# Optimization experiments

Hardware: AMD Instinct MI355X
Metric: run time of the kernel (lower is better)

The kernel has to match this reference:

```python
import jax, jax.numpy as jnp
import numpy as np

BINS = 100
ALPHA = 0.1

def entropy_batch(h):
    # Faithful to torch: histogram path is detached (done in numpy in original).
    h = jax.lax.stop_gradient(h)
    B, D = h.shape
    hp = h - jnp.min(h, axis=1, keepdims=True)
    hn = hp / jnp.max(hp, axis=1, keepdims=True)  # normalized to [0, 1]
    # np.histogram with `bins` uniform bins over [0,1]; rightmost edge inclusive -> clip
    idx = jnp.clip(jnp.floor(hn * BINS).astype(jnp.int32), 0, BINS - 1)
    rows = jnp.arange(B)[:, None]
    counts = jnp.zeros((B, BINS), jnp.float32).at[rows, idx].add(1.0)
    px = counts / jnp.float32(D)
    safe = jnp.where(px > 0, px, 1.0)
    ent = -jnp.sum(px * jnp.log(safe), axis=1) + jnp.log(jnp.float32(BINS))
    return jnp.mean(ent)

def setup_inputs() -> dict:
    key = jax.random.key(0)
    ks = jax.random.split(key, 8)
    B = 65536
    archi = [246, 246, 246, 246, 246, 246]
    dims = [784] + archi
    inp = {"x": jax.random.normal(ks[0], (B, 1, 28, 28), jnp.float32)}
    for i in range(6):
        inp[f"W{i+1}"] = 0.01 * jax.random.normal(ks[i + 1], (dims[i + 1], dims[i]), jnp.float32)
        inp[f"b{i+1}"] = jnp.zeros((dims[i + 1],), jnp.float32)
    inp["W7"] = 0.01 * jax.random.normal(ks[7], (10, archi[-1]), jnp.float32)
    inp["b7"] = jnp.zeros((10,), jnp.float32)
    return inp

def reference(x, W1, b1, W2, b2, W3, b3, W4, b4, W5, b5, W6, b6, W7, b7):
    h = x.reshape(-1, 784)
    Hs = []
    for W, b in ((W1, b1), (W2, b2), (W3, b3), (W4, b4), (W5, b5), (W6, b6)):
        h = jax.nn.leaky_relu(h @ W.T + b, negative_slope=ALPHA)
        Hs.append(entropy_batch(h))
    logits = jax.nn.relu(h @ W7.T + b7)
    out = jax.nn.log_softmax(logits, axis=1)
    return (out, Hs[0], Hs[1], Hs[2], Hs[3], Hs[4], Hs[5])
```

## Files before the change

kernel.cpp:

```cpp
#include <hip/hip_runtime.h>
#include <cstdint>
#include <cmath>

#define BATCH 65536
#define NREAL 246
#define NPAD  256
#define K1    784
#define K1PAD 832
#define BINS  100
#define ALPHA 0.1f
#define RB    32
#define NBLK  (BATCH/RB)

typedef __bf16 bf16x8 __attribute__((ext_vector_type(8)));
typedef __bf16 bf16x4 __attribute__((ext_vector_type(4)));
typedef float  f32x4  __attribute__((ext_vector_type(4)));

#define OFF_HS     0
#define OFF_STAGE  16384
#define OFF_HIST   16384
#define OFF_MN     29184
#define OFF_MX     29696
#define OFF_LUT    30208
#define OFF_WENT   31232
#define LDS_TOTAL  31328

__global__ __launch_bounds__(256)
void pad_weights(const float* __restrict__ W1, const float* __restrict__ W2,
                 const float* __restrict__ W3, const float* __restrict__ W4,
                 const float* __restrict__ W5, const float* __restrict__ W6,
                 const float* __restrict__ W7,
                 __bf16* __restrict__ W1p, __bf16* __restrict__ Wp,
                 __bf16* __restrict__ W7p)
{
    int tid = blockIdx.x * 256 + threadIdx.x;
    const int n1 = NPAD * K1PAD;
    const int n2 = 5 * NPAD * NPAD;
    if (tid < n1) {
        int row = tid / K1PAD;
        int k   = tid - row * K1PAD;
        W1p[tid] = (__bf16)((row < NREAL && k < K1) ? W1[row * K1 + k] : 0.0f);
    } else if (tid < n1 + n2) {
        int t = tid - n1;
        int wsel = t >> 16;
        int idx  = t & 65535;
        int row  = idx >> 8, k = idx & 255;
        const float* W = (wsel == 0) ? W2 : (wsel == 1) ? W3 : (wsel == 2) ? W4
                        : (wsel == 3) ? W5 : W6;
        Wp[t] = (__bf16)((row < NREAL && k < NREAL) ? W[row * NREAL + k] : 0.0f);
    } else if (tid < n1 + n2 + 16 * NPAD) {
        int t = tid - n1 - n2;
        int row = t >> 8, k = t & 255;
        W7p[t] = (__bf16)((row < 10 && k < NREAL) ? W7[row * NREAL + k] : 0.0f);
    }
}

__global__ __launch_bounds__(256)
void mega(const float* __restrict__ x,
          const __bf16* __restrict__ W1p,
          const __bf16* __restrict__ Wp,
          const __bf16* __restrict__ W7p,
          const float* __restrict__ b1, const float* __restrict__ b2,
          const float* __restrict__ b3, const float* __restrict__ b4,
          const float* __restrict__ b5, const float* __restrict__ b6,
          const float* __restrict__ b7,
          float* __restrict__ out, float* __restrict__ partial)
{
    __shared__ char smem[LDS_TOTAL];
    char*  Hb    = smem + OFF_HS;
    float* rowmn = (float*)(smem + OFF_MN);
    float* rowmx = (float*)(smem + OFF_MX);
    float* lut   = (float*)(smem + OFF_LUT);
    float* went  = (float*)(smem + OFF_WENT);

    const int tid = threadIdx.x;
    const int w = tid >> 6, l = tid & 63;
    const int lane16 = l & 15, lane4 = l >> 4;
    const int m0 = blockIdx.x * RB;

    if (tid > 0 && tid < 247) lut[tid] = (float)tid * logf((float)tid);
    if (tid == 0) lut[0] = 0.0f;

    f32x4 acc[2][4];
#pragma unroll
    for (int i = 0; i < 2; ++i)
#pragma unroll
        for (int j = 0; j < 4; ++j) acc[i][j] = f32x4{0.f, 0.f, 0.f, 0.f};

    auto loadBh = [&](bf16x8 (&dst)[4], const __bf16* Bbase, int Kb, int kt, int kk) {
        const __bf16* p = Bbase + (size_t)(w * 64 + lane16) * Kb + kt * 64 + kk * 32 + lane4 * 8;
#pragma unroll
        for (int j = 0; j < 4; ++j)
            dst[j] = *(const bf16x8*)(p + (size_t)j * 16 * Kb);
    };

    auto computeHalf = [&](const char* Ab, int rowStride, int kbyte, const bf16x8 (&bfr)[4]) {
#pragma unroll
        for (int i = 0; i < 2; ++i) {
            int row = i * 16 + lane16;
            bf16x8 af = *(const bf16x8*)(Ab + row * rowStride + ((kbyte + lane4 * 16) ^ ((row & 7) << 4)));
            __builtin_amdgcn_s_setprio(1);
#pragma unroll
            for (int j = 0; j < 4; ++j)
                acc[i][j] = __builtin_amdgcn_mfma_f32_16x16x32_bf16(af, bfr[j], acc[i][j], 0, 0, 0);
            __builtin_amdgcn_s_setprio(0);
        }
    };

    auto epilogue = [&](const float* bias) {
        float bv[4];
#pragma unroll
        for (int j = 0; j < 4; ++j) {
            int col = w * 64 + j * 16 + lane16;
            bv[j] = (col < NREAL) ? bias[col] : 0.0f;
        }
#pragma unroll
        for (int i = 0; i < 2; ++i) {
#pragma unroll
            for (int rr = 0; rr < 4; ++rr) {
                int row = i * 16 + lane4 * 4 + rr;
                int swz = (row & 7) << 4;
                float mn = 1e30f, mx = -1e30f;
#pragma unroll
                for (int j = 0; j < 4; ++j) {
                    int col = w * 64 + j * 16 + lane16;
                    bool cv = col < NREAL;
                    float v = acc[i][j][rr] + bv[j];
                    v = v > 0.0f ? v : ALPHA * v;
                    *(__bf16*)(Hb + row * 512 + ((col * 2) ^ swz)) = cv ? (__bf16)v : (__bf16)0.0f;
                    mn = fminf(mn, cv ? v : 1e30f);
                    mx = fmaxf(mx, cv ? v : -1e30f);
                }
#pragma unroll
                for (int off = 1; off < 16; off <<= 1) {
                    mn = fminf(mn, __shfl_xor(mn, off, 64));
                    mx = fmaxf(mx, __shfl_xor(mx, off, 64));
                }
                if (lane16 == 0) {
                    rowmn[row * 4 + w] = mn;
                    rowmx[row * 4 + w] = mx;
                }
            }
        }
    };

    auto entropy = [&](int li) {
        int* histW = (int*)(smem + OFF_HIST) + w * 800;
        const int rg = l >> 3;
        const int q  = l & 7;
        const int row = w * 8 + rg;
        f32x4 m4 = *(const f32x4*)(rowmn + row * 4);
        f32x4 x4 = *(const f32x4*)(rowmx + row * 4);
        float mn = fminf(fminf(m4[0], m4[1]), fminf(m4[2], m4[3]));
        float mx = fmaxf(fmaxf(x4[0], x4[1]), fmaxf(x4[2], x4[3]));
        float rgv = mx - mn;
        float rs = (rgv > 0.0f) ? 100.0f / rgv : 0.0f;
#pragma unroll
        for (int t = 0; t < 13; ++t) { int b = t * 64 + l; if (b < 800) histW[b] = 0; }
        asm volatile("s_waitcnt lgkmcnt(0)" ::: "memory");
        const int swz = (row & 7) << 4;
#pragma unroll
        for (int t = 0; t < 8; ++t) {
            int c0 = q * 32 + t * 4;
            bf16x4 hv = *(const bf16x4*)(Hb + row * 512 + ((c0 * 2) ^ swz));
#pragma unroll
            for (int e = 0; e < 4; ++e) {
                if (c0 + e < NREAL) {
                    int idx = (int)floorf(((float)hv[e] - mn) * rs);
                    idx = idx < 0 ? 0 : (idx > BINS - 1 ? BINS - 1 : idx);
                    atomicAdd(&histW[rg * 100 + idx], 1);
                }
            }
        }
        asm volatile("s_waitcnt lgkmcnt(0)" ::: "memory");
        float S = 0.0f;
        const int rbase = rg * 100, tb = q * 13;
#pragma unroll
        for (int t = 0; t < 13; ++t) {
            int b = tb + t;
            if (b < 100) S += lut[histW[rbase + b]];
        }
#pragma unroll
        for (int off = 1; off < 64; off <<= 1) S += __shfl_xor(S, off, 64);
        if (l == 0) went[w * 6 + li] = 8.0f * logf(246.0f) - S * (1.0f / 246.0f);
    };

    bf16x8 curB[4], nxtB[4];

    {
        const int srow = tid >> 3;
        const int skc  = (tid & 7) * 8;
        float4 xr0, xr1;
        auto issueX = [&](int kt) {
            int k0 = kt * 64 + skc;
            if (k0 < K1) {
                const float* gx = x + (size_t)(m0 + srow) * K1 + k0;
                xr0 = *(const float4*)gx;
                xr1 = *(const float4*)(gx + 4);
            } else {
                xr0 = float4{0.f,0.f,0.f,0.f};
                xr1 = float4{0.f,0.f,0.f,0.f};
            }
        };
        auto writeX = [&](int buf) {
            bf16x8 h;
            h[0]=(__bf16)xr0.x; h[1]=(__bf16)xr0.y; h[2]=(__bf16)xr0.z; h[3]=(__bf16)xr0.w;
            h[4]=(__bf16)xr1.x; h[5]=(__bf16)xr1.y; h[6]=(__bf16)xr1.z; h[7]=(__bf16)xr1.w;
            char* st = smem + OFF_STAGE + buf * 4096;
            *(bf16x8*)(st + srow * 128 + ((skc * 2) ^ ((srow & 7) << 4))) = h;
        };

        issueX(0);
        writeX(0);
        issueX(1);
        loadBh(curB, W1p, K1PAD, 0, 0);
        for (int kt = 0; kt < 13; ++kt) {
            __syncthreads();
            if (kt < 12) {
                writeX((kt + 1) & 1);
                if (kt < 11) issueX(kt + 2);
            }
            const char* st = smem + OFF_STAGE + (kt & 1) * 4096;
            loadBh(nxtB, W1p, K1PAD, kt, 1);
            computeHalf(st, 128, 0, curB);
            if (kt < 12) loadBh(curB, W1p, K1PAD, kt + 1, 0);
            computeHalf(st, 128, 64, nxtB);
        }
    }

    loadBh(curB, Wp, NPAD, 0, 0);
    epilogue(b1);
    __syncthreads();
    entropy(0);

    const float* bsel[5] = {b2, b3, b4, b5, b6};
    for (int li = 0; li < 5; ++li) {
        const __bf16* Bp = Wp + (size_t)li * (NPAD * NPAD);
#pragma unroll
        for (int i = 0; i < 2; ++i)
#pragma unroll
            for (int j = 0; j < 4; ++j) acc[i][j] = f32x4{0.f, 0.f, 0.f, 0.f};

#pragma unroll
        for (int kt = 0; kt < 4; ++kt) {
            loadBh(nxtB, Bp, NPAD, kt, 1);
            computeHalf(Hb, 512, kt * 128, curB);
            if (kt < 3)      loadBh(curB, Bp, NPAD, kt + 1, 0);
            else if (li < 4) loadBh(curB, Bp + NPAD * NPAD, NPAD, 0, 0);
            computeHalf(Hb, 512, kt * 128 + 64, nxtB);
        }

        __syncthreads();
        epilogue(bsel[li]);
        __syncthreads();
        entropy(li + 1);
    }

    if (w < 2) {
        f32x4 hacc = f32x4{0.f, 0.f, 0.f, 0.f};
        int row = w * 16 + lane16;
#pragma unroll
        for (int kt = 0; kt < 8; ++kt) {
            bf16x8 af = *(const bf16x8*)(Hb + row * 512 + ((kt * 64 + lane4 * 16) ^ ((row & 7) << 4)));
            bf16x8 bf = *(const bf16x8*)(W7p + (size_t)lane16 * NPAD + kt * 32 + lane4 * 8);
            hacc = __builtin_amdgcn_mfma_f32_16x16x32_bf16(af, bf, hacc, 0, 0, 0);
        }
        float bv = (lane16 < 10) ? b7[lane16] : 0.0f;
#pragma unroll
        for (int r = 0; r < 4; ++r) {
            float lg = fmaxf(hacc[r] + bv, 0.0f);
            float vm = (lane16 < 10) ? lg : -1e30f;
#pragma unroll
            for (int off = 8; off; off >>= 1) vm = fmaxf(vm, __shfl_xor(vm, off, 64));
            float ex = (lane16 < 10) ? expf(lg - vm) : 0.0f;
#pragma unroll
            for (int off = 8; off; off >>= 1) ex += __shfl_xor(ex, off, 64);
            float ls = vm + logf(ex);
            if (lane16 < 10) {
                int grow = m0 + w * 16 + lane4 * 4 + r;
                out[(size_t)grow * 10 + lane16] = lg - ls;
            }
        }
    }

    __syncthreads();
    if (tid < 6) {
        float s = 0.0f;
#pragma unroll
        for (int q = 0; q < 4; ++q) s += went[q * 6 + tid];
        partial[tid * NBLK + blockIdx.x] = s;
    }
}

__global__ __launch_bounds__(256)
void reduce_kernel(const float* __restrict__ partial, float* __restrict__ out)
{
    __shared__ float s[256];
    const int li = blockIdx.x, tid = threadIdx.x;
    float a = 0.0f;
    for (int i = tid; i < NBLK; i += 256) a += partial[li * NBLK + i];
    s[tid] = a;
    __syncthreads();
    for (int st = 128; st; st >>= 1) {
        if (tid < st) s[tid] += s[tid + st];
        __syncthreads();
    }
    if (tid == 0)
        out[(size_t)BATCH * 10 + li] = s[0] / (float)BATCH + logf((float)BINS);
}

extern "C" void kernel_launch(void* const* d_in, const int* in_sizes, int n_in,
                              void* d_out, int out_size, void* d_ws, size_t ws_size,
                              hipStream_t stream)
{
    (void)in_sizes; (void)n_in; (void)out_size; (void)ws_size;

    const float* x  = (const float*)d_in[0];
    const float* W1 = (const float*)d_in[1];
    const float* b1 = (const float*)d_in[2];
    const float* W2 = (const float*)d_in[3];
    const float* b2 = (const float*)d_in[4];
    const float* W3 = (const float*)d_in[5];
    const float* b3 = (const float*)d_in[6];
    const float* W4 = (const float*)d_in[7];
    const float* b4 = (const float*)d_in[8];
    const float* W5 = (const float*)d_in[9];
    const float* b5 = (const float*)d_in[10];
    const float* W6 = (const float*)d_in[11];
    const float* b6 = (const float*)d_in[12];
    const float* W7 = (const float*)d_in[13];
    const float* b7 = (const float*)d_in[14];

    char* ws = (char*)d_ws;
    __bf16* W1p = (__bf16*)(ws);
    __bf16* Wp  = (__bf16*)(ws + 425984);
    __bf16* W7p = (__bf16*)(ws + 1081344);
    float*  partial = (float*)(ws + 1089536);
    float*  out = (float*)d_out;

    pad_weights<<<2128, 256, 0, stream>>>(W1, W2, W3, W4, W5, W6, W7, W1p, Wp, W7p);
    mega<<<NBLK, 256, 0, stream>>>(x, W1p, Wp, W7p, b1, b2, b3, b4, b5, b6, b7, out, partial);
    reduce_kernel<<<6, 256, 0, stream>>>(partial, out);
}
```

Before: 325.7 us.

## Transpose MFMA output so epilogue writes vector rows and histograms from registers

Swaps the MFMA operands so each lane holds four consecutive columns of one row. The epilogue can then write bf16x4 vectors to LDS and reduce min/max with two shuffles instead of four. The histogram is now filled directly from the fp32 accumulators in registers rather than by re-reading the bf16 LDS activations, and biases are padded into one workspace array so they load as vectors. In exchange it adds an extra barrier per layer. Binning on fp32 values instead of bf16-rounded values may shift some bin assignments.

```diff
diff --git a/kernel.cpp b/kernel.cpp
--- a/kernel.cpp
+++ b/kernel.cpp
@@ -30,12 +30,16 @@
                  const float* __restrict__ W3, const float* __restrict__ W4,
                  const float* __restrict__ W5, const float* __restrict__ W6,
                  const float* __restrict__ W7,
+                 const float* __restrict__ b1, const float* __restrict__ b2,
+                 const float* __restrict__ b3, const float* __restrict__ b4,
+                 const float* __restrict__ b5, const float* __restrict__ b6,
                  __bf16* __restrict__ W1p, __bf16* __restrict__ Wp,
-                 __bf16* __restrict__ W7p)
+                 __bf16* __restrict__ W7p, float* __restrict__ bpad)
 {
     int tid = blockIdx.x * 256 + threadIdx.x;
     const int n1 = NPAD * K1PAD;
     const int n2 = 5 * NPAD * NPAD;
+    const int n3 = 16 * NPAD;
     if (tid < n1) {
         int row = tid / K1PAD;
         int k   = tid - row * K1PAD;
@@ -48,10 +52,16 @@
         const float* W = (wsel == 0) ? W2 : (wsel == 1) ? W3 : (wsel == 2) ? W4
                         : (wsel == 3) ? W5 : W6;
         Wp[t] = (__bf16)((row < NREAL && k < NREAL) ? W[row * NREAL + k] : 0.0f);
-    } else if (tid < n1 + n2 + 16 * NPAD) {
+    } else if (tid < n1 + n2 + n3) {
         int t = tid - n1 - n2;
         int row = t >> 8, k = t & 255;
         W7p[t] = (__bf16)((row < 10 && k < NREAL) ? W7[row * NREAL + k] : 0.0f);
+    } else if (tid < n1 + n2 + n3 + 6 * NPAD) {
+        int t = tid - n1 - n2 - n3;
+        int li = t >> 8, k = t & 255;
+        const float* b = (li == 0) ? b1 : (li == 1) ? b2 : (li == 2) ? b3
+                        : (li == 3) ? b4 : (li == 4) ? b5 : b6;
+        bpad[t] = (k < NREAL) ? b[k] : 0.0f;
     }
 }
 
@@ -60,9 +70,7 @@
           const __bf16* __restrict__ W1p,
           const __bf16* __restrict__ Wp,
           const __bf16* __restrict__ W7p,
-          const float* __restrict__ b1, const float* __restrict__ b2,
-          const float* __restrict__ b3, const float* __restrict__ b4,
-          const float* __restrict__ b5, const float* __restrict__ b6,
+          const float* __restrict__ bpad,
           const float* __restrict__ b7,
           float* __restrict__ out, float* __restrict__ partial)
 {
@@ -72,6 +80,7 @@
     float* rowmx = (float*)(smem + OFF_MX);
     float* lut   = (float*)(smem + OFF_LUT);
     float* went  = (float*)(smem + OFF_WENT);
+    int*   hist  = (int*)(smem + OFF_HIST);
 
     const int tid = threadIdx.x;
     const int w = tid >> 6, l = tid & 63;
@@ -102,83 +111,87 @@
             __builtin_amdgcn_s_setprio(1);
 #pragma unroll
             for (int j = 0; j < 4; ++j)
-                acc[i][j] = __builtin_amdgcn_mfma_f32_16x16x32_bf16(af, bfr[j], acc[i][j], 0, 0, 0);
+                acc[i][j] = __builtin_amdgcn_mfma_f32_16x16x32_bf16(bfr[j], af, acc[i][j], 0, 0, 0);
             __builtin_amdgcn_s_setprio(0);
         }
     };
 
-    auto epilogue = [&](const float* bias) {
-        float bv[4];
-#pragma unroll
-        for (int j = 0; j < 4; ++j) {
-            int col = w * 64 + j * 16 + lane16;
-            bv[j] = (col < NREAL) ? bias[col] : 0.0f;
-        }
+    auto epilogue = [&](const float* bp) {
+        f32x4 bq[4];
+#pragma unroll
+        for (int j = 0; j < 4; ++j)
+            bq[j] = *(const f32x4*)(bp + w * 64 + j * 16 + lane4 * 4);
 #pragma unroll
         for (int i = 0; i < 2; ++i) {
-#pragma unroll
-            for (int rr = 0; rr < 4; ++rr) {
-                int row = i * 16 + lane4 * 4 + rr;
-                int swz = (row & 7) << 4;
-                float mn = 1e30f, mx = -1e30f;
-#pragma unroll
-                for (int j = 0; j < 4; ++j) {
-                    int col = w * 64 + j * 16 + lane16;
-                    bool cv = col < NREAL;
-                    float v = acc[i][j][rr] + bv[j];
+            const int m = i * 16 + lane16;
+            const int swz = (m & 7) << 4;
+            float mn = 1e30f, mx = -1e30f;
+#pragma unroll
+            for (int j = 0; j < 4; ++j) {
+                const int nbase = w * 64 + j * 16 + lane4 * 4;
+                bf16x4 hv;
+#pragma unroll
+                for (int r = 0; r < 4; ++r) {
+                    float v = acc[i][j][r] + bq[j][r];
                     v = v > 0.0f ? v : ALPHA * v;
-                    *(__bf16*)(Hb + row * 512 + ((col * 2) ^ swz)) = cv ? (__bf16)v : (__bf16)0.0f;
-                    mn = fminf(mn, cv ? v : 1e30f);
-                    mx = fmaxf(mx, cv ? v : -1e30f);
+                    bool valid = (nbase + r) < NREAL;
+                    hv[r] = valid ? (__bf16)v : (__bf16)0.0f;
+                    acc[i][j][r] = v;
+                    mn = fminf(mn, valid ? v : 1e30f);
+                    mx = fmaxf(mx, valid ? v : -1e30f);
                 }
-#pragma unroll
-                for (int off = 1; off < 16; off <<= 1) {
-                    mn = fminf(mn, __shfl_xor(mn, off, 64));
-                    mx = fmaxf(mx, __shfl_xor(mx, off, 64));
+                *(bf16x4*)(Hb + m * 512 + ((nbase * 2) ^ swz)) = hv;
+            }
+            mn = fminf(mn, __shfl_xor(mn, 16, 64));
+            mx = fmaxf(mx, __shfl_xor(mx, 16, 64));
+            mn = fminf(mn, __shfl_xor(mn, 32, 64));
+            mx = fmaxf(mx, __shfl_xor(mx, 32, 64));
+            if (lane4 == 0) {
+                rowmn[m * 4 + w] = mn;
+                rowmx[m * 4 + w] = mx;
+            }
+        }
+    };
+
+    auto ezero = [&]() {
+        int4* hz = (int4*)hist;
+        const int4 z = int4{0, 0, 0, 0};
+        hz[tid] = z; hz[tid + 256] = z; hz[tid + 512] = z;
+        if (tid < 32) hz[tid + 768] = z;
+    };
+    auto efill = [&]() {
+#pragma unroll
+        for (int i = 0; i < 2; ++i) {
+            const int m = i * 16 + lane16;
+            f32x4 m4 = *(const f32x4*)(rowmn + m * 4);
+            f32x4 x4 = *(const f32x4*)(rowmx + m * 4);
+            float mn = fminf(fminf(m4[0], m4[1]), fminf(m4[2], m4[3]));
+            float mx = fmaxf(fmaxf(x4[0], x4[1]), fmaxf(x4[2], x4[3]));
+            float rgv = mx - mn;
+            float rs = (rgv > 0.0f) ? 100.0f / rgv : 0.0f;
+            int* hrow = hist + m * 100;
+#pragma unroll
+            for (int j = 0; j < 4; ++j) {
+                const int nbase = w * 64 + j * 16 + lane4 * 4;
+#pragma unroll
+                for (int r = 0; r < 4; ++r) {
+                    if (nbase + r < NREAL) {
+                        int idx = (int)floorf((acc[i][j][r] - mn) * rs);
+                        idx = idx < 0 ? 0 : (idx > BINS - 1 ? BINS - 1 : idx);
+                        atomicAdd(&hrow[idx], 1);
+                    }
                 }
-                if (lane16 == 0) {
-                    rowmn[row * 4 + w] = mn;
-                    rowmx[row * 4 + w] = mx;
-                }
-            }
-        }
-    };
-
-    auto entropy = [&](int li) {
-        int* histW = (int*)(smem + OFF_HIST) + w * 800;
-        const int rg = l >> 3;
-        const int q  = l & 7;
+            }
+        }
+    };
+    auto esum = [&](int li) {
+        const int rg = l >> 3, q = l & 7;
         const int row = w * 8 + rg;
-        f32x4 m4 = *(const f32x4*)(rowmn + row * 4);
-        f32x4 x4 = *(const f32x4*)(rowmx + row * 4);
-        float mn = fminf(fminf(m4[0], m4[1]), fminf(m4[2], m4[3]));
-        float mx = fmaxf(fmaxf(x4[0], x4[1]), fmaxf(x4[2], x4[3]));
-        float rgv = mx - mn;
-        float rs = (rgv > 0.0f) ? 100.0f / rgv : 0.0f;
-#pragma unroll
-        for (int t = 0; t < 13; ++t) { int b = t * 64 + l; if (b < 800) histW[b] = 0; }
-        asm volatile("s_waitcnt lgkmcnt(0)" ::: "memory");
-        const int swz = (row & 7) << 4;
-#pragma unroll
-        for (int t = 0; t < 8; ++t) {
-            int c0 = q * 32 + t * 4;
-            bf16x4 hv = *(const bf16x4*)(Hb + row * 512 + ((c0 * 2) ^ swz));
-#pragma unroll
-            for (int e = 0; e < 4; ++e) {
-                if (c0 + e < NREAL) {
-                    int idx = (int)floorf(((float)hv[e] - mn) * rs);
-                    idx = idx < 0 ? 0 : (idx > BINS - 1 ? BINS - 1 : idx);
-                    atomicAdd(&histW[rg * 100 + idx], 1);
-                }
-            }
-        }
-        asm volatile("s_waitcnt lgkmcnt(0)" ::: "memory");
         float S = 0.0f;
-        const int rbase = rg * 100, tb = q * 13;
 #pragma unroll
         for (int t = 0; t < 13; ++t) {
-            int b = tb + t;
-            if (b < 100) S += lut[histW[rbase + b]];
+            int b = q * 13 + t;
+            if (b < 100) S += lut[hist[row * 100 + b]];
         }
 #pragma unroll
         for (int off = 1; off < 64; off <<= 1) S += __shfl_xor(S, off, 64);
@@ -229,11 +242,14 @@
     }
 
     loadBh(curB, Wp, NPAD, 0, 0);
-    epilogue(b1);
-    __syncthreads();
-    entropy(0);
-
-    const float* bsel[5] = {b2, b3, b4, b5, b6};
+    epilogue(bpad);
+    __syncthreads();
+    ezero();
+    __syncthreads();
+    efill();
+    __syncthreads();
+    esum(0);
+
     for (int li = 0; li < 5; ++li) {
         const __bf16* Bp = Wp + (size_t)li * (NPAD * NPAD);
 #pragma unroll
@@ -251,9 +267,12 @@
         }
 
         __syncthreads();
-        epilogue(bsel[li]);
+        ezero();
+        epilogue(bpad + (li + 1) * NPAD);
         __syncthreads();
-        entropy(li + 1);
+        efill();
+        __syncthreads();
+        esum(li + 1);
     }
 
     if (w < 2) {
@@ -335,10 +354,13 @@
     __bf16* W1p = (__bf16*)(ws);
     __bf16* Wp  = (__bf16*)(ws + 425984);
     __bf16* W7p = (__bf16*)(ws + 1081344);
-    float*  partial = (float*)(ws + 1089536);
+    float*  bpad = (float*)(ws + 1089536);
+    float*  partial = (float*)(ws + 1095680);
     float*  out = (float*)d_out;
 
-    pad_weights<<<2128, 256, 0, stream>>>(W1, W2, W3, W4, W5, W6, W7, W1p, Wp, W7p);
-    mega<<<NBLK, 256, 0, stream>>>(x, W1p, Wp, W7p, b1, b2, b3, b4, b5, b6, b7, out, partial);
+    pad_weights<<<2134, 256, 0, stream>>>(W1, W2, W3, W4, W5, W6, W7,
+                                          b1, b2, b3, b4, b5, b6,
+                                          W1p, Wp, W7p, bpad);
+    mega<<<NBLK, 256, 0, stream>>>(x, W1p, Wp, W7p, bpad, b7, out, partial);
     reduce_kernel<<<6, 256, 0, stream>>>(partial, out);
 }
```

Result: faster. 297.3 us (-8.7%).
